# Optimization experiments

Hardware: AMD Instinct MI355X
Metric: run time of the kernel (lower is better)

The kernel has to match this reference:

```python
import jax, jax.numpy as jnp
import numpy as np

D_MODEL, NHEAD = 1024, 16
DK = D_MODEL // NHEAD


def setup_inputs() -> dict:
    key = jax.random.key(0)
    ks = jax.random.split(key, 10)
    B, T = 2, 2048
    s = 1.0 / np.sqrt(D_MODEL)
    inp = {
        "x": jax.random.normal(ks[0], (B, T, D_MODEL), dtype=jnp.float32),
        "attn_bias": jax.random.normal(ks[1], (1, NHEAD, T, T), dtype=jnp.float32),
        "Wq": jax.random.normal(ks[2], (D_MODEL, D_MODEL), dtype=jnp.float32) * s,
        "bq": jnp.zeros((D_MODEL,), dtype=jnp.float32),
        "Wk": jax.random.normal(ks[3], (D_MODEL, D_MODEL), dtype=jnp.float32) * s,
        "bk": jnp.zeros((D_MODEL,), dtype=jnp.float32),
        "Wv": jax.random.normal(ks[4], (D_MODEL, D_MODEL), dtype=jnp.float32) * s,
        "bv": jnp.zeros((D_MODEL,), dtype=jnp.float32),
        "Wo": jax.random.normal(ks[5], (D_MODEL, D_MODEL), dtype=jnp.float32) * s,
        "bo": jnp.zeros((D_MODEL,), dtype=jnp.float32),
    }
    return inp


def reference(x, attn_bias, Wq, bq, Wk, bk, Wv, bv, Wo, bo):
    B, T, D = x.shape
    H, dk = NHEAD, DK
    # torch Linear: y = x @ W.T + b
    q = (x @ Wq.T + bq).reshape(B, T, H, dk).transpose(0, 2, 1, 3)  # [B,H,T,dk]
    k = (x @ Wk.T + bk).reshape(B, T, H, dk).transpose(0, 2, 1, 3)
    v = (x @ Wv.T + bv).reshape(B, T, H, dk).transpose(0, 2, 1, 3)
    scores = jnp.einsum("bhqd,bhkd->bhqk", q, k) / jnp.sqrt(jnp.float32(dk))
    scores = scores + attn_bias  # broadcast over batch
    attn = jax.nn.softmax(scores, axis=-1)  # dropout p=0.0 -> identity
    out = jnp.einsum("bhqk,bhkd->bhqd", attn, v)
    out = out.transpose(0, 2, 1, 3).reshape(B, T, D)
    return out @ Wo.T + bo
```

## Files before the change

kernel.cpp:

```cpp
#include <hip/hip_runtime.h>

typedef unsigned short u16;
typedef unsigned int u32;
using short8 = __attribute__((ext_vector_type(8))) short;
using f32x4  = __attribute__((ext_vector_type(4))) float;

#define D_MODEL 1024
#define NHEAD 16
#define DKV 64
#define TSEQ 2048
#define BATCH 2
#define L2E 1.44269504f
#define CSHIFT 12.0f

#define GLOAD16(gp, lp)                                                      \
    __builtin_amdgcn_global_load_lds(                                        \
        (const __attribute__((address_space(1))) u32*)(gp),                  \
        (__attribute__((address_space(3))) u32*)(lp), 16, 0, 0)

__device__ __forceinline__ u16 f2bf(float f) {
    union { float f; u32 i; } c; c.f = f;
    u32 x = c.i;
    return (u16)((x + 0x7FFFu + ((x >> 16) & 1u)) >> 16);
}
__device__ __forceinline__ u16 f2bf_fast(float f) {
    union { float f; u32 i; } c; c.f = f;
    return (u16)((c.i + 0x8000u) >> 16);
}

__global__ __launch_bounds__(256) void prep_cvt(
    const float* __restrict__ x,  const float* __restrict__ Wq,
    const float* __restrict__ Wk, const float* __restrict__ Wv,
    const float* __restrict__ Wo, u16* __restrict__ dst)
{
    size_t e = ((size_t)blockIdx.x * 256 + threadIdx.x) * 8;
    const float* src; size_t off;
    if (e < 4194304u)      { src = x;  off = e; }
    else if (e < 5242880u) { src = Wq; off = e - 4194304u; }
    else if (e < 6291456u) { src = Wk; off = e - 5242880u; }
    else if (e < 7340032u) { src = Wv; off = e - 6291456u; }
    else                   { src = Wo; off = e - 7340032u; }
    float4 a = *(const float4*)(src + off);
    float4 b = *(const float4*)(src + off + 4);
    short8 v;
    v[0] = (short)f2bf(a.x); v[1] = (short)f2bf(a.y);
    v[2] = (short)f2bf(a.z); v[3] = (short)f2bf(a.w);
    v[4] = (short)f2bf(b.x); v[5] = (short)f2bf(b.y);
    v[6] = (short)f2bf(b.z); v[7] = (short)f2bf(b.w);
    *(short8*)(dst + e) = v;
}

__global__ __launch_bounds__(256) void qkv_gemm(
    const u16* __restrict__ xbf, const u16* __restrict__ wbf,
    const float* __restrict__ bq, const float* __restrict__ bk,
    const float* __restrict__ bv, u16* __restrict__ qkv)
{
    __shared__ __align__(16) u16 Alds[128 * 64];
    __shared__ __align__(16) u16 Blds[128 * 64];

    const int fid = blockIdx.x;
    const int xcd = fid & 7, ii = fid >> 3;
    const int z = ii >> 5, r2 = ii & 31;
    const int nb = r2 & 7, mb = xcd * 4 + (r2 >> 3);
    const int n0 = nb * 128, m0 = mb * 128;
    const u16* W = wbf + (size_t)z * 1048576;
    const float* bias = (z == 0) ? bq : (z == 1) ? bk : bv;
    u16* out = qkv + (size_t)z * 4194304;

    const int t = threadIdx.x;
    const int wave = t >> 6, lane = t & 63, l15 = lane & 15, quad = lane >> 4;
    const int wm = (wave >> 1) * 64, wn = (wave & 1) * 64;

    f32x4 acc[4][4];
#pragma unroll
    for (int i = 0; i < 4; ++i)
#pragma unroll
        for (int j = 0; j < 4; ++j)
#pragma unroll
            for (int r = 0; r < 4; ++r) acc[i][j][r] = 0.f;

    const int rs = t >> 3, cs = (t & 7) * 8;
    const u16* ga = xbf + (size_t)(m0 + rs) * 1024 + cs;
    const u16* gb = W   + (size_t)(n0 + rs) * 1024 + cs;
    u16* la = &Alds[rs * 64 + cs];
    u16* lb = &Blds[rs * 64 + cs];

    for (int kt = 0; kt < 16; ++kt) {
        const int k0 = kt * 64;
#pragma unroll
        for (int c = 0; c < 4; ++c) {
            GLOAD16(ga + (size_t)(c * 32) * 1024 + k0, la + c * 32 * 64);
            GLOAD16(gb + (size_t)(c * 32) * 1024 + k0, lb + c * 32 * 64);
        }
        __syncthreads();
#pragma unroll
        for (int ki = 0; ki < 2; ++ki) {
            short8 af[4], bfr[4];
#pragma unroll
            for (int i = 0; i < 4; ++i)
                af[i] = *(const short8*)&Alds[(wm + i * 16 + l15) * 64 + ki * 32 + quad * 8];
#pragma unroll
            for (int j = 0; j < 4; ++j)
                bfr[j] = *(const short8*)&Blds[(wn + j * 16 + l15) * 64 + ki * 32 + quad * 8];
#pragma unroll
            for (int i = 0; i < 4; ++i)
#pragma unroll
                for (int j = 0; j < 4; ++j)
                    acc[i][j] = __builtin_amdgcn_mfma_f32_16x16x32_bf16(af[i], bfr[j], acc[i][j], 0, 0, 0);
        }
        __syncthreads();
    }

#pragma unroll
    for (int j = 0; j < 4; ++j) {
        int n = n0 + wn + j * 16 + l15;
        float bb = bias[n];
        int h = n >> 6, d = n & 63;
#pragma unroll
        for (int i = 0; i < 4; ++i)
#pragma unroll
            for (int r = 0; r < 4; ++r) {
                int m = m0 + wm + i * 16 + quad * 4 + r;
                int bidx = m >> 11, tt = m & 2047;
                out[(((size_t)(bidx * NHEAD + h)) * TSEQ + tt) * DKV + d] =
                    f2bf(acc[i][j][r] + bb);
            }
    }
}

__global__ __launch_bounds__(512, 4) void attn_kernel(
    const u16* __restrict__ qws, const u16* __restrict__ kws, const u16* __restrict__ vws,
    const float* __restrict__ bias, u16* __restrict__ ows)
{
    __shared__ __align__(16) u16 Klds[2][64 * 64];
    __shared__ __align__(16) u16 Vt[2][2][64 * 72];
    __shared__ __align__(16) u16 Plds[2][64 * 72];

    const int fid = blockIdx.x;
    const int xcd = fid & 7, ii = fid >> 3;
    const int h = xcd * 2 + (ii >> 5);
    const int qt = ii & 31;
    const int q0 = qt * 64;

    const int t = threadIdx.x;
    const int bg = t >> 8;
    const int tl = t & 255;
    const int wave = tl >> 6, lane = tl & 63, l15 = lane & 15, quad = lane >> 4;
    const int bh = bg * NHEAD + h;
    const size_t bhoff = (size_t)bh * TSEQ * DKV;

    short8 qa0, qa1;
    {
        const u16* qp = qws + bhoff + (size_t)(q0 + wave * 16 + l15) * DKV;
        qa0 = *(const short8*)(qp + quad * 8);
        qa1 = *(const short8*)(qp + 32 + quad * 8);
    }

    float l_run[4] = {0.f, 0.f, 0.f, 0.f};
    f32x4 o_acc[4];
#pragma unroll
    for (int db = 0; db < 4; ++db)
#pragma unroll
        for (int r = 0; r < 4; ++r) o_acc[db][r] = 0.f;

    const float* bias_h = bias + ((size_t)h * TSEQ + q0) * TSEQ;
    const int a8 = tl & 7, c8 = a8 * 8, rp = tl >> 3;
    const int rbase = wave * 16 + quad * 4;
    const int sw8 = l15 & 7;
    const int vbk = rp >> 2;
    const int vkcl = (2 * rp) & 7;

    const u16* kpbase = kws + bhoff + (size_t)rp * DKV + ((a8 ^ (rp & 7)) * 8);
    const u16* vpbase = vws + bhoff + (size_t)(2 * rp) * DKV + c8;
    u16* kl = &Klds[bg][rp * 64 + c8];

    GLOAD16(kpbase, kl);
    GLOAD16(kpbase + 32 * DKV, kl + 32 * 64);
    {
        short8 v0 = *(const short8*)vpbase;
        short8 v1 = *(const short8*)(vpbase + DKV);
        u16* vtb = &Vt[bg][0][0];
#pragma unroll
        for (int j = 0; j < 8; ++j) {
            int d = c8 + j;
            u32 val = ((u32)(u16)v0[j]) | (((u32)(u16)v1[j]) << 16);
            *(u32*)&vtb[d * 72 + ((vbk ^ a8) * 8) + vkcl] = val;
        }
    }
    float bz[16];
#pragma unroll
    for (int cb = 0; cb < 4; ++cb)
#pragma unroll
        for (int r = 0; r < 4; ++r)
            bz[cb * 4 + r] = bias_h[(size_t)(rbase + r) * TSEQ + cb * 16 + l15];
    __syncthreads();

    for (int kt = 0; kt < TSEQ / 64; ++kt) {
        const int cur = kt & 1;

        f32x4 s[4];
#pragma unroll
        for (int cb = 0; cb < 4; ++cb)
#pragma unroll
            for (int r = 0; r < 4; ++r) s[cb][r] = 0.f;
#pragma unroll
        for (int cb = 0; cb < 4; ++cb) {
            const u16* kr = &Klds[bg][(cb * 16 + l15) * 64];
            short8 kb0 = *(const short8*)(kr + ((quad ^ sw8) * 8));
            short8 kb1 = *(const short8*)(kr + (((quad + 4) ^ sw8) * 8));
            s[cb] = __builtin_amdgcn_mfma_f32_16x16x32_bf16(qa0, kb0, s[cb], 0, 0, 0);
            s[cb] = __builtin_amdgcn_mfma_f32_16x16x32_bf16(qa1, kb1, s[cb], 0, 0, 0);
        }

        __syncthreads();

        const int ktn = (kt < 31) ? kt + 1 : kt;
        const size_t koff = (size_t)ktn * 64 * DKV;
        GLOAD16(kpbase + koff, kl);
        GLOAD16(kpbase + koff + 32 * DKV, kl + 32 * 64);
        short8 v0n = *(const short8*)(vpbase + koff);
        short8 v1n = *(const short8*)(vpbase + koff + DKV);
        float bzn[16];
#pragma unroll
        for (int cb = 0; cb < 4; ++cb)
#pragma unroll
            for (int r = 0; r < 4; ++r)
                bzn[cb * 4 + r] =
                    bias_h[(size_t)(rbase + r) * TSEQ + ktn * 64 + cb * 16 + l15];

#pragma unroll
        for (int cb = 0; cb < 4; ++cb)
#pragma unroll
            for (int r = 0; r < 4; ++r) {
                float arg = fmaf(s[cb][r], 0.125f * L2E,
                                 fmaf(bz[cb * 4 + r], L2E, -CSHIFT * L2E));
                float p = exp2f(arg);
                l_run[r] += p;
                Plds[bg][(rbase + r) * 72 + cb * 16 + l15] = f2bf_fast(p);
            }

        {
            const u16* pr = &Plds[bg][(wave * 16 + l15) * 72 + quad * 8];
            short8 pa0 = *(const short8*)pr;
            short8 pa1 = *(const short8*)(pr + 32);
            const u16* vtc = &Vt[bg][cur][0];
#pragma unroll
            for (int db = 0; db < 4; ++db) {
                int d = db * 16 + l15;
                int sw = (d >> 3) & 7;
                const u16* vr = &vtc[d * 72];
                short8 vb0 = *(const short8*)(vr + ((quad ^ sw) * 8));
                short8 vb1 = *(const short8*)(vr + (((4 + quad) ^ sw) * 8));
                o_acc[db] = __builtin_amdgcn_mfma_f32_16x16x32_bf16(pa0, vb0, o_acc[db], 0, 0, 0);
                o_acc[db] = __builtin_amdgcn_mfma_f32_16x16x32_bf16(pa1, vb1, o_acc[db], 0, 0, 0);
            }
        }

        {
            u16* vtb = &Vt[bg][cur ^ 1][0];
#pragma unroll
            for (int j = 0; j < 8; ++j) {
                int d = c8 + j;
                u32 val = ((u32)(u16)v0n[j]) | (((u32)(u16)v1n[j]) << 16);
                *(u32*)&vtb[d * 72 + ((vbk ^ a8) * 8) + vkcl] = val;
            }
        }
#pragma unroll
        for (int i = 0; i < 16; ++i) bz[i] = bzn[i];

        __syncthreads();
    }

#pragma unroll
    for (int r = 0; r < 4; ++r) {
        float v = l_run[r];
        v += __shfl_xor(v, 1);
        v += __shfl_xor(v, 2);
        v += __shfl_xor(v, 4);
        v += __shfl_xor(v, 8);
        l_run[r] = v;
    }
#pragma unroll
    for (int r = 0; r < 4; ++r) {
        float inv = 1.f / l_run[r];
        int row = q0 + rbase + r;
#pragma unroll
        for (int db = 0; db < 4; ++db)
            ows[bhoff + (size_t)row * DKV + db * 16 + l15] = f2bf(o_acc[db][r] * inv);
    }
}

__global__ __launch_bounds__(256) void out_gemm(
    const u16* __restrict__ ows, const u16* __restrict__ wobf,
    const float* __restrict__ bo, float* __restrict__ out)
{
    __shared__ __align__(16) u16 Alds[128 * 64];
    __shared__ __align__(16) u16 Blds[64 * 64];

    const int fid = blockIdx.x;
    const int xcd = fid & 7, ii = fid >> 3;
    const int nb = ii & 15, mb = xcd * 4 + (ii >> 4);
    const int n0 = nb * 64, m0 = mb * 128;

    const int t = threadIdx.x;
    const int wave = t >> 6, lane = t & 63, l15 = lane & 15, quad = lane >> 4;
    const int wm = (wave >> 1) * 64, wn = (wave & 1) * 32;

    f32x4 acc[4][2];
#pragma unroll
    for (int i = 0; i < 4; ++i)
#pragma unroll
        for (int j = 0; j < 2; ++j)
#pragma unroll
            for (int r = 0; r < 4; ++r) acc[i][j][r] = 0.f;

    const int rs = t >> 3, cs = (t & 7) * 8;
    const int bidx = m0 >> 11, tt0 = m0 & 2047;
    const u16* gaBase = ows + (((size_t)(bidx * NHEAD)) * TSEQ + tt0 + rs) * DKV + cs;
    const u16* gb = wobf + (size_t)(n0 + rs) * 1024 + cs;
    u16* la = &Alds[rs * 64 + cs];
    u16* lb = &Blds[rs * 64 + cs];

    for (int kt = 0; kt < 16; ++kt) {
        const int k0 = kt * 64;
#pragma unroll
        for (int c = 0; c < 4; ++c)
            GLOAD16(gaBase + ((size_t)kt * TSEQ + c * 32) * DKV, la + c * 32 * 64);
#pragma unroll
        for (int c = 0; c < 2; ++c)
            GLOAD16(gb + (size_t)(c * 32) * 1024 + k0, lb + c * 32 * 64);
        __syncthreads();
#pragma unroll
        for (int ki = 0; ki < 2; ++ki) {
            short8 af[4], bfr[2];
#pragma unroll
            for (int i = 0; i < 4; ++i)
                af[i] = *(const short8*)&Alds[(wm + i * 16 + l15) * 64 + ki * 32 + quad * 8];
#pragma unroll
            for (int j = 0; j < 2; ++j)
                bfr[j] = *(const short8*)&Blds[(wn + j * 16 + l15) * 64 + ki * 32 + quad * 8];
#pragma unroll
            for (int i = 0; i < 4; ++i)
#pragma unroll
                for (int j = 0; j < 2; ++j)
                    acc[i][j] = __builtin_amdgcn_mfma_f32_16x16x32_bf16(af[i], bfr[j], acc[i][j], 0, 0, 0);
        }
        __syncthreads();
    }

#pragma unroll
    for (int j = 0; j < 2; ++j) {
        int n = n0 + wn + j * 16 + l15;
        float bb = bo[n];
#pragma unroll
        for (int i = 0; i < 4; ++i)
#pragma unroll
            for (int r = 0; r < 4; ++r) {
                int m = m0 + wm + i * 16 + quad * 4 + r;
                out[(size_t)m * 1024 + n] = acc[i][j][r] + bb;
            }
    }
}

extern "C" void kernel_launch(void* const* d_in, const int* in_sizes, int n_in,
                              void* d_out, int out_size, void* d_ws, size_t ws_size,
                              hipStream_t stream)
{
    const float* x  = (const float*)d_in[0];
    const float* ab = (const float*)d_in[1];
    const float* Wq = (const float*)d_in[2];
    const float* bq = (const float*)d_in[3];
    const float* Wk = (const float*)d_in[4];
    const float* bk = (const float*)d_in[5];
    const float* Wv = (const float*)d_in[6];
    const float* bv = (const float*)d_in[7];
    const float* Wo = (const float*)d_in[8];
    const float* bo = (const float*)d_in[9];
    float* out = (float*)d_out;

    u16* wsu = (u16*)d_ws;
    const size_t WBF = 4194304;
    const size_t QKV = 8388608;
    const size_t OWS = 20971520;
    const size_t QSZ = 4194304;

    prep_cvt<<<4096, 256, 0, stream>>>(x, Wq, Wk, Wv, Wo, wsu);
    qkv_gemm<<<768, 256, 0, stream>>>(wsu, wsu + WBF, bq, bk, bv, wsu + QKV);
    attn_kernel<<<512, 512, 0, stream>>>(wsu + QKV, wsu + QKV + QSZ,
                                         wsu + QKV + 2 * QSZ, ab, wsu + OWS);
    out_gemm<<<512, 256, 0, stream>>>(wsu + OWS, wsu + WBF + 3 * 1048576, bo, out);
}
```

Before: 505.5 us.

## Rework attention kernel to 32x32x16 MFMA tiles with 128-row query blocks

The attention kernel moves from 16x16x32 MFMA to 32x32x16 MFMA, with each wave now owning 32 query rows instead of 16. Each block covers 128 query rows of one batch-head with 256 threads, replacing 64 rows for both batches with 512 threads. Each K/V tile loaded into LDS is therefore reused across twice as many query rows per wave, which cuts LDS traffic and instruction count per FLOP. In exchange, register pressure rises (32 bias values, 16-element accumulators), launch bounds drop to 2 blocks per CU, and bias loads become more strided per lane.

```diff
diff --git a/kernel.cpp b/kernel.cpp
--- a/kernel.cpp
+++ b/kernel.cpp
@@ -4,6 +4,7 @@
 typedef unsigned int u32;
 using short8 = __attribute__((ext_vector_type(8))) short;
 using f32x4  = __attribute__((ext_vector_type(4))) float;
+using f32x16 = __attribute__((ext_vector_type(16))) float;
 
 #define D_MODEL 1024
 #define NHEAD 16
@@ -128,58 +129,57 @@
     }
 }
 
-__global__ __launch_bounds__(512, 4) void attn_kernel(
+__global__ __launch_bounds__(256, 2) void attn_kernel(
     const u16* __restrict__ qws, const u16* __restrict__ kws, const u16* __restrict__ vws,
     const float* __restrict__ bias, u16* __restrict__ ows)
 {
-    __shared__ __align__(16) u16 Klds[2][64 * 64];
-    __shared__ __align__(16) u16 Vt[2][2][64 * 72];
-    __shared__ __align__(16) u16 Plds[2][64 * 72];
+    __shared__ __align__(16) u16 Klds[64 * 64];
+    __shared__ __align__(16) u16 Vt[2][64 * 72];
+    __shared__ __align__(16) u16 Plds[4 * 32 * 72];
 
     const int fid = blockIdx.x;
     const int xcd = fid & 7, ii = fid >> 3;
-    const int h = xcd * 2 + (ii >> 5);
-    const int qt = ii & 31;
-    const int q0 = qt * 64;
+    const int bh = xcd * 4 + (ii >> 4);
+    const int qt = ii & 15;
+    const int h = bh & 15;
 
     const int t = threadIdx.x;
-    const int bg = t >> 8;
-    const int tl = t & 255;
-    const int wave = tl >> 6, lane = tl & 63, l15 = lane & 15, quad = lane >> 4;
-    const int bh = bg * NHEAD + h;
+    const int wave = t >> 6, lane = t & 63, l31 = lane & 31, h5 = lane >> 5;
+    const int qw = qt * 128 + wave * 32;
     const size_t bhoff = (size_t)bh * TSEQ * DKV;
 
-    short8 qa0, qa1;
+    short8 qa[4];
     {
-        const u16* qp = qws + bhoff + (size_t)(q0 + wave * 16 + l15) * DKV;
-        qa0 = *(const short8*)(qp + quad * 8);
-        qa1 = *(const short8*)(qp + 32 + quad * 8);
-    }
-
-    float l_run[4] = {0.f, 0.f, 0.f, 0.f};
-    f32x4 o_acc[4];
-#pragma unroll
-    for (int db = 0; db < 4; ++db)
-#pragma unroll
-        for (int r = 0; r < 4; ++r) o_acc[db][r] = 0.f;
-
-    const float* bias_h = bias + ((size_t)h * TSEQ + q0) * TSEQ;
-    const int a8 = tl & 7, c8 = a8 * 8, rp = tl >> 3;
-    const int rbase = wave * 16 + quad * 4;
-    const int sw8 = l15 & 7;
-    const int vbk = rp >> 2;
-    const int vkcl = (2 * rp) & 7;
+        const u16* qp = qws + bhoff + (size_t)(qw + l31) * DKV + h5 * 8;
+#pragma unroll
+        for (int dc = 0; dc < 4; ++dc)
+            qa[dc] = *(const short8*)(qp + dc * 16);
+    }
+
+    float l_run[16];
+#pragma unroll
+    for (int r = 0; r < 16; ++r) l_run[r] = 0.f;
+    f32x16 oacc[2];
+#pragma unroll
+    for (int dn = 0; dn < 2; ++dn)
+#pragma unroll
+        for (int r = 0; r < 16; ++r) oacc[dn][r] = 0.f;
+
+    const float* bias_h = bias + ((size_t)h * TSEQ + qw) * TSEQ;
+    const int a8 = t & 7, c8 = a8 * 8, rp = t >> 3;
+    const int vbk = rp >> 2, vkcl = (2 * rp) & 7;
+    const int wbase = wave * (32 * 72);
 
     const u16* kpbase = kws + bhoff + (size_t)rp * DKV + ((a8 ^ (rp & 7)) * 8);
     const u16* vpbase = vws + bhoff + (size_t)(2 * rp) * DKV + c8;
-    u16* kl = &Klds[bg][rp * 64 + c8];
+    u16* kl = &Klds[rp * 64 + c8];
 
     GLOAD16(kpbase, kl);
     GLOAD16(kpbase + 32 * DKV, kl + 32 * 64);
     {
         short8 v0 = *(const short8*)vpbase;
         short8 v1 = *(const short8*)(vpbase + DKV);
-        u16* vtb = &Vt[bg][0][0];
+        u16* vtb = &Vt[0][0];
 #pragma unroll
         for (int j = 0; j < 8; ++j) {
             int d = c8 + j;
@@ -187,29 +187,31 @@
             *(u32*)&vtb[d * 72 + ((vbk ^ a8) * 8) + vkcl] = val;
         }
     }
-    float bz[16];
-#pragma unroll
-    for (int cb = 0; cb < 4; ++cb)
-#pragma unroll
-        for (int r = 0; r < 4; ++r)
-            bz[cb * 4 + r] = bias_h[(size_t)(rbase + r) * TSEQ + cb * 16 + l15];
+    float bz[32];
+#pragma unroll
+    for (int kn = 0; kn < 2; ++kn)
+#pragma unroll
+        for (int r = 0; r < 16; ++r)
+            bz[kn * 16 + r] =
+                bias_h[(size_t)((r & 3) + 8 * (r >> 2) + 4 * h5) * TSEQ + kn * 32 + l31];
     __syncthreads();
 
     for (int kt = 0; kt < TSEQ / 64; ++kt) {
         const int cur = kt & 1;
 
-        f32x4 s[4];
-#pragma unroll
-        for (int cb = 0; cb < 4; ++cb)
-#pragma unroll
-            for (int r = 0; r < 4; ++r) s[cb][r] = 0.f;
-#pragma unroll
-        for (int cb = 0; cb < 4; ++cb) {
-            const u16* kr = &Klds[bg][(cb * 16 + l15) * 64];
-            short8 kb0 = *(const short8*)(kr + ((quad ^ sw8) * 8));
-            short8 kb1 = *(const short8*)(kr + (((quad + 4) ^ sw8) * 8));
-            s[cb] = __builtin_amdgcn_mfma_f32_16x16x32_bf16(qa0, kb0, s[cb], 0, 0, 0);
-            s[cb] = __builtin_amdgcn_mfma_f32_16x16x32_bf16(qa1, kb1, s[cb], 0, 0, 0);
+        f32x16 s[2];
+#pragma unroll
+        for (int kn = 0; kn < 2; ++kn)
+#pragma unroll
+            for (int r = 0; r < 16; ++r) s[kn][r] = 0.f;
+#pragma unroll
+        for (int dc = 0; dc < 4; ++dc) {
+#pragma unroll
+            for (int kn = 0; kn < 2; ++kn) {
+                short8 kb = *(const short8*)
+                    &Klds[(kn * 32 + l31) * 64 + (((dc * 2 + h5) ^ (l31 & 7)) * 8)];
+                s[kn] = __builtin_amdgcn_mfma_f32_32x32x16_bf16(qa[dc], kb, s[kn], 0, 0, 0);
+            }
         }
 
         __syncthreads();
@@ -220,44 +222,41 @@
         GLOAD16(kpbase + koff + 32 * DKV, kl + 32 * 64);
         short8 v0n = *(const short8*)(vpbase + koff);
         short8 v1n = *(const short8*)(vpbase + koff + DKV);
-        float bzn[16];
-#pragma unroll
-        for (int cb = 0; cb < 4; ++cb)
-#pragma unroll
-            for (int r = 0; r < 4; ++r)
-                bzn[cb * 4 + r] =
-                    bias_h[(size_t)(rbase + r) * TSEQ + ktn * 64 + cb * 16 + l15];
-
-#pragma unroll
-        for (int cb = 0; cb < 4; ++cb)
-#pragma unroll
-            for (int r = 0; r < 4; ++r) {
-                float arg = fmaf(s[cb][r], 0.125f * L2E,
-                                 fmaf(bz[cb * 4 + r], L2E, -CSHIFT * L2E));
+        float bzn[32];
+#pragma unroll
+        for (int kn = 0; kn < 2; ++kn)
+#pragma unroll
+            for (int r = 0; r < 16; ++r)
+                bzn[kn * 16 + r] =
+                    bias_h[(size_t)((r & 3) + 8 * (r >> 2) + 4 * h5) * TSEQ +
+                           ktn * 64 + kn * 32 + l31];
+
+#pragma unroll
+        for (int kn = 0; kn < 2; ++kn)
+#pragma unroll
+            for (int r = 0; r < 16; ++r) {
+                float arg = fmaf(s[kn][r], 0.125f * L2E,
+                                 fmaf(bz[kn * 16 + r], L2E, -CSHIFT * L2E));
                 float p = exp2f(arg);
                 l_run[r] += p;
-                Plds[bg][(rbase + r) * 72 + cb * 16 + l15] = f2bf_fast(p);
-            }
+                int row = (r & 3) + 8 * (r >> 2) + 4 * h5;
+                Plds[wbase + row * 72 + kn * 32 + l31] = f2bf_fast(p);
+            }
+
+#pragma unroll
+        for (int kc = 0; kc < 4; ++kc) {
+            short8 pa = *(const short8*)&Plds[wbase + l31 * 72 + kc * 16 + h5 * 8];
+#pragma unroll
+            for (int dn = 0; dn < 2; ++dn) {
+                int d = dn * 32 + l31;
+                short8 vb = *(const short8*)
+                    &Vt[cur][d * 72 + (((kc * 2 + h5) ^ ((d >> 3) & 7)) * 8)];
+                oacc[dn] = __builtin_amdgcn_mfma_f32_32x32x16_bf16(pa, vb, oacc[dn], 0, 0, 0);
+            }
+        }
 
         {
-            const u16* pr = &Plds[bg][(wave * 16 + l15) * 72 + quad * 8];
-            short8 pa0 = *(const short8*)pr;
-            short8 pa1 = *(const short8*)(pr + 32);
-            const u16* vtc = &Vt[bg][cur][0];
-#pragma unroll
-            for (int db = 0; db < 4; ++db) {
-                int d = db * 16 + l15;
-                int sw = (d >> 3) & 7;
-                const u16* vr = &vtc[d * 72];
-                short8 vb0 = *(const short8*)(vr + ((quad ^ sw) * 8));
-                short8 vb1 = *(const short8*)(vr + (((4 + quad) ^ sw) * 8));
-                o_acc[db] = __builtin_amdgcn_mfma_f32_16x16x32_bf16(pa0, vb0, o_acc[db], 0, 0, 0);
-                o_acc[db] = __builtin_amdgcn_mfma_f32_16x16x32_bf16(pa1, vb1, o_acc[db], 0, 0, 0);
-            }
-        }
-
-        {
-            u16* vtb = &Vt[bg][cur ^ 1][0];
+            u16* vtb = &Vt[cur ^ 1][0];
 #pragma unroll
             for (int j = 0; j < 8; ++j) {
                 int d = c8 + j;
@@ -266,27 +265,24 @@
             }
         }
 #pragma unroll
-        for (int i = 0; i < 16; ++i) bz[i] = bzn[i];
-
-        __syncthreads();
-    }
-
-#pragma unroll
-    for (int r = 0; r < 4; ++r) {
+        for (int i = 0; i < 32; ++i) bz[i] = bzn[i];
+
+        __syncthreads();
+    }
+
+#pragma unroll
+    for (int r = 0; r < 16; ++r) {
         float v = l_run[r];
         v += __shfl_xor(v, 1);
         v += __shfl_xor(v, 2);
         v += __shfl_xor(v, 4);
         v += __shfl_xor(v, 8);
-        l_run[r] = v;
-    }
-#pragma unroll
-    for (int r = 0; r < 4; ++r) {
-        float inv = 1.f / l_run[r];
-        int row = q0 + rbase + r;
-#pragma unroll
-        for (int db = 0; db < 4; ++db)
-            ows[bhoff + (size_t)row * DKV + db * 16 + l15] = f2bf(o_acc[db][r] * inv);
+        v += __shfl_xor(v, 16);
+        float inv = 1.f / v;
+        int row = qw + (r & 3) + 8 * (r >> 2) + 4 * h5;
+#pragma unroll
+        for (int dn = 0; dn < 2; ++dn)
+            ows[bhoff + (size_t)row * DKV + dn * 32 + l31] = f2bf(oacc[dn][r] * inv);
     }
 }
 
@@ -386,7 +382,7 @@
 
     prep_cvt<<<4096, 256, 0, stream>>>(x, Wq, Wk, Wv, Wo, wsu);
     qkv_gemm<<<768, 256, 0, stream>>>(wsu, wsu + WBF, bq, bk, bv, wsu + QKV);
-    attn_kernel<<<512, 512, 0, stream>>>(wsu + QKV, wsu + QKV + QSZ,
+    attn_kernel<<<512, 256, 0, stream>>>(wsu + QKV, wsu + QKV + QSZ,
                                          wsu + QKV + 2 * QSZ, ab, wsu + OWS);
     out_gemm<<<512, 256, 0, stream>>>(wsu + OWS, wsu + WBF + 3 * 1048576, bo, out);
 }
```

Measured after the change: 503.8 us. No clear change (-0.3%).
